# Optimization experiments

Hardware: AMD Instinct MI355X
Metric: run time of the kernel (lower is better)

## Reference

```python
import jax, jax.numpy as jnp
import numpy as np

N = 100000      # nodes
E = 1600000     # edges (before self-loops)
IN = 128        # in_channels
HID = 16        # hidden per head
HEADS = 8
OUT = 16        # out_channels (classes)
NEG_SLOPE = 0.2


def setup_inputs() -> dict:
    key = jax.random.key(0)
    ks = jax.random.split(key, 10)
    x = jax.random.normal(ks[0], (N, IN), jnp.float32)
    edge_index = jax.random.randint(ks[1], (2, E), 0, N, jnp.int32)
    g = lambda k, shape, fan: (jax.random.normal(k, shape, jnp.float32)
                               * (1.0 / np.sqrt(fan)).astype(np.float32))
    # layer 1: in -> heads*hid
    W1 = g(ks[2], (IN, HEADS * HID), IN)
    att_src1 = g(ks[3], (HEADS, HID), HID)
    att_dst1 = g(ks[4], (HEADS, HID), HID)
    b1 = jnp.zeros((HEADS * HID,), jnp.float32)
    # layer 2: heads*hid -> out, 1 head, concat=False
    W2 = g(ks[5], (HEADS * HID, OUT), HEADS * HID)
    att_src2 = g(ks[6], (1, OUT), OUT)
    att_dst2 = g(ks[7], (1, OUT), OUT)
    b2 = jnp.zeros((OUT,), jnp.float32)
    return dict(x=x, edge_index=edge_index, W1=W1, att_src1=att_src1,
                att_dst1=att_dst1, b1=b1, W2=W2, att_src2=att_src2,
                att_dst2=att_dst2, b2=b2)


def gat_conv(x, src, dst, W, a_src, a_dst, b, concat):
    """PyG-style GATConv (eval mode). src->dst message flow."""
    num_nodes = x.shape[0]
    H, C = a_src.shape
    h = (x @ W).reshape(num_nodes, H, C)                      # [N,H,C]
    # per-node attention halves, gathered to edges
    e = (h * a_src).sum(-1)[src] + (h * a_dst).sum(-1)[dst]   # [Etot,H]
    e = jax.nn.leaky_relu(e, NEG_SLOPE)
    # segment softmax over edges grouped by destination node
    emax = jax.ops.segment_max(e, dst, num_segments=num_nodes)    # [N,H]
    ee = jnp.exp(e - emax[dst])
    denom = jax.ops.segment_sum(ee, dst, num_segments=num_nodes)  # [N,H]
    alpha = ee / (denom[dst] + 1e-16)                              # [Etot,H]
    # weighted scatter-aggregate of source features
    msg = h[src] * alpha[:, :, None]                               # [Etot,H,C]
    out = jax.ops.segment_sum(msg, dst, num_segments=num_nodes)    # [N,H,C]
    out = out.reshape(num_nodes, H * C) if concat else out.mean(axis=1)
    return out + b


def reference(x, edge_index, W1, att_src1, att_dst1, b1,
              W2, att_src2, att_dst2, b2):
    # add self loops (PyG GATConv default)
    loop = jnp.arange(N, dtype=edge_index.dtype)
    src = jnp.concatenate([edge_index[0], loop])
    dst = jnp.concatenate([edge_index[1], loop])

    h = gat_conv(x, src, dst, W1, att_src1, att_dst1, b1, concat=True)
    embeddings = jax.nn.elu(h)
    logits = gat_conv(embeddings, src, dst, W2, att_src2, att_dst2, b2,
                      concat=False)
    return jax.nn.log_softmax(logits, axis=1), embeddings
```

## Files before the change

kernel.cpp:

```cpp
#include <hip/hip_runtime.h>
#include <hip/hip_bf16.h>
#include <math.h>

#define N_NODES 100000
#define E_EDGES 1600000
#define ETOT    (E_EDGES + N_NODES)
#define NEG     0.2f

#define SH        8
#define NBUCK     ((N_NODES + 255) >> 8)
#define BIN_TILE  4096
#define NBIN      ((E_EDGES + BIN_TILE - 1) / BIN_TILE)
#define CAP_B     5120

#define NMFMA     ((N_NODES + 63) / 64)
#define G_A       782
#define G_B       (NMFMA - G_A)

typedef __attribute__((ext_vector_type(8))) short bf16x8;
typedef __attribute__((ext_vector_type(4))) float f32x4;
typedef __attribute__((ext_vector_type(2))) short bf16p;

__device__ inline float lrelu(float x) { return x > 0.f ? x : NEG * x; }
__device__ inline float bflo(unsigned int b) { return __uint_as_float(b << 16); }
__device__ inline float bfhi(unsigned int b) { return __uint_as_float(b & 0xFFFF0000u); }
__device__ inline unsigned short f2bf(float f) {
    unsigned int u = __float_as_uint(f);
    return (unsigned short)((u + 0x7FFFu + ((u >> 16) & 1u)) >> 16);
}

__device__ inline float dot2bf(unsigned int wp, unsigned int hp, float c) {
#if __has_builtin(__builtin_amdgcn_fdot2_f32_bf16)
    return __builtin_amdgcn_fdot2_f32_bf16(__builtin_bit_cast(bf16p, wp),
                                           __builtin_bit_cast(bf16p, hp),
                                           c, false);
#else
    return fmaf(bflo(wp), bflo(hp), fmaf(bfhi(wp), bfhi(hp), c));
#endif
}

__global__ __launch_bounds__(256) void k_wt(const float* __restrict__ W,
                                            unsigned short* __restrict__ wtg) {
    int t = blockIdx.x * 256 + threadIdx.x;
    if (t >= 128 * 128) return;
    int n = t >> 7, k = t & 127;
    wtg[t] = f2bf(W[k * 128 + n]);
}

__global__ __launch_bounds__(256) void k_pack(const float* __restrict__ s1,
                                              unsigned short* __restrict__ s1b) {
    int n = blockIdx.x * 256 + threadIdx.x;
    if (n >= N_NODES) return;
    const float4* p = (const float4*)(s1 + (size_t)n * 8);
    float4 a = p[0], b = p[1];
    union { unsigned short u[8]; uint4 v; } o;
    o.u[0] = f2bf(a.x); o.u[1] = f2bf(a.y); o.u[2] = f2bf(a.z); o.u[3] = f2bf(a.w);
    o.u[4] = f2bf(b.x); o.u[5] = f2bf(b.y); o.u[6] = f2bf(b.z); o.u[7] = f2bf(b.w);
    *(uint4*)(s1b + (size_t)n * 8) = o.v;
}

__device__ __forceinline__ void gemm1_role(
    int n0, int t, unsigned short (*xb)[136],
    const float* __restrict__ x, const unsigned short* __restrict__ wtg,
    const float* __restrict__ asrc, const float* __restrict__ adst,
    __hip_bfloat16* __restrict__ h1b, float* __restrict__ s1,
    float* __restrict__ d1) {
#pragma unroll
    for (int i = 0; i < 8; ++i) {
        int i4 = t + i * 256;
        int r = i4 >> 5;
        int c = (i4 & 31) * 4;
        float4 v = make_float4(0.f, 0.f, 0.f, 0.f);
        if (n0 + r < N_NODES) v = *(const float4*)(x + (size_t)(n0 + r) * 128 + c);
        xb[r][c + 0] = f2bf(v.x);
        xb[r][c + 1] = f2bf(v.y);
        xb[r][c + 2] = f2bf(v.z);
        xb[r][c + 3] = f2bf(v.w);
    }
    __syncthreads();

    int l = t & 63, wv = t >> 6;
    int col = l & 15, q4 = l >> 4;
    int rbase = wv * 16;
    int koff = q4 * 8;

    bf16x8 a[4];
#pragma unroll
    for (int st = 0; st < 4; ++st)
        a[st] = *(const bf16x8*)&xb[rbase + col][st * 32 + koff];

    int nodeb = n0 + rbase + q4 * 4;
#pragma unroll
    for (int nt = 0; nt < 8; ++nt) {
        f32x4 acc = {0.f, 0.f, 0.f, 0.f};
        const unsigned short* wrow = wtg + (size_t)(nt * 16 + col) * 128 + koff;
#pragma unroll
        for (int st = 0; st < 4; ++st) {
            bf16x8 b = *(const bf16x8*)(wrow + st * 32);
            acc = __builtin_amdgcn_mfma_f32_16x16x32_bf16(a[st], b, acc, 0, 0, 0);
        }
        float as_v = asrc[nt * 16 + col];
        float ad_v = adst[nt * 16 + col];
#pragma unroll
        for (int r = 0; r < 4; ++r) {
            int node = nodeb + r;
            if (node < N_NODES)
                h1b[(size_t)node * 128 + nt * 16 + col] = __float2bfloat16(acc[r]);
            float ps = acc[r] * as_v, pd = acc[r] * ad_v;
#pragma unroll
            for (int ofs = 1; ofs < 16; ofs <<= 1) {
                ps += __shfl_xor(ps, ofs, 64);
                pd += __shfl_xor(pd, ofs, 64);
            }
            if (col == 0 && node < N_NODES) {
                s1[node * 8 + nt] = ps;
                d1[node * 8 + nt] = pd;
            }
        }
    }
}

union SmemBin {
    struct {
        int2 st[BIN_TILE];
        int  hist[NBUCK + 1];
        int  lstart[NBUCK];
        int  gbase[NBUCK];
        int  tsum[256];
    } b;
    unsigned short xb[64][136];
};

__global__ __launch_bounds__(256) void k_parBin(
    const int* __restrict__ src, const int* __restrict__ dst,
    int* __restrict__ gcur, int2* __restrict__ coo,
    const float* __restrict__ x, const unsigned short* __restrict__ wtg,
    const float* __restrict__ asrc, const float* __restrict__ adst,
    __hip_bfloat16* __restrict__ h1b, float* __restrict__ s1,
    float* __restrict__ d1) {
    __shared__ SmemBin sm;
    int bid = blockIdx.x, t = threadIdx.x;
    bool isBin = (bid % 3 == 0) && (bid / 3 < NBIN);
    if (!isBin) {
        int gid = bid - bid / 3 - 1;
        gemm1_role(gid * 64, t, sm.xb, x, wtg, asrc, adst, h1b, s1, d1);
        return;
    }
    int wb = bid / 3;
    int e0 = wb * BIN_TILE;
    int nE = min(BIN_TILE, E_EDGES - e0);
    for (int i = t; i <= NBUCK; i += 256) sm.b.hist[i] = 0;
    __syncthreads();
    for (int i = t; i < nE; i += 256)
        atomicAdd(&sm.b.hist[dst[e0 + i] >> SH], 1);
    __syncthreads();
    int i0 = 2 * t, i1 = 2 * t + 1;
    int h0 = (i0 < NBUCK) ? sm.b.hist[i0] : 0;
    int h1v = (i1 < NBUCK) ? sm.b.hist[i1] : 0;
    int s = h0 + h1v;
    sm.b.tsum[t] = s;
    __syncthreads();
    for (int ofs = 1; ofs < 256; ofs <<= 1) {
        int u = (t >= ofs) ? sm.b.tsum[t - ofs] : 0;
        __syncthreads();
        sm.b.tsum[t] += u;
        __syncthreads();
    }
    int pre = sm.b.tsum[t] - s;
    if (i0 < NBUCK) sm.b.hist[i0] = pre;
    if (i1 < NBUCK) sm.b.hist[i1] = pre + h0;
    if (t == 255) sm.b.hist[NBUCK] = sm.b.tsum[255];
    __syncthreads();
    for (int i = t; i < NBUCK; i += 256) {
        int st_ = sm.b.hist[i];
        int cnt = sm.b.hist[i + 1] - st_;
        sm.b.lstart[i] = st_;
        if (cnt > 0) sm.b.gbase[i] = i * CAP_B + atomicAdd(&gcur[i], cnt);
    }
    __syncthreads();
    for (int i = t; i < nE; i += 256) {
        int sv = src[e0 + i], dv = dst[e0 + i];
        int p = atomicAdd(&sm.b.hist[dv >> SH], 1);
        sm.b.st[p] = make_int2(sv, dv);
    }
    __syncthreads();
    for (int i = t; i < nE; i += 256) {
        int2 e = sm.b.st[i];
        int b2 = e.y >> SH;
        int slot = sm.b.gbase[b2] + (i - sm.b.lstart[b2]);
        slot = min(slot, (b2 + 1) * CAP_B - 1);
        coo[slot] = e;
    }
}

__global__ __launch_bounds__(256) void k_scanb(const int* __restrict__ gcur,
                                               int* __restrict__ bbase,
                                               int* __restrict__ off) {
    __shared__ int tsum[256];
    int t = threadIdx.x;
    int i0 = 2 * t, i1 = 2 * t + 1;
    int a = 0, b = 0;
    if (i0 < NBUCK) a = min(gcur[i0], CAP_B) + min(256, N_NODES - (i0 << SH));
    if (i1 < NBUCK) b = min(gcur[i1], CAP_B) + min(256, N_NODES - (i1 << SH));
    int s = a + b;
    tsum[t] = s;
    __syncthreads();
    for (int ofs = 1; ofs < 256; ofs <<= 1) {
        int u = (t >= ofs) ? tsum[t - ofs] : 0;
        __syncthreads();
        tsum[t] += u;
        __syncthreads();
    }
    int pre = tsum[t] - s;
    if (i0 < NBUCK) bbase[i0] = pre;
    if (i1 < NBUCK) bbase[i1] = pre + a;
    if (t == 0) off[N_NODES] = ETOT;
}

union SmemFine {
    struct {
        int ldeg[256];
        int lpre[256];
        int lsrc[CAP_B + 256];
    } f;
    unsigned short xb[64][136];
};

__global__ __launch_bounds__(256) void k_parFine(
    const int2* __restrict__ coo, const int* __restrict__ gcur,
    const int* __restrict__ bbase, int* __restrict__ off,
    int* __restrict__ csr,
    const float* __restrict__ x, const unsigned short* __restrict__ wtg,
    const float* __restrict__ asrc, const float* __restrict__ adst,
    __hip_bfloat16* __restrict__ h1b, float* __restrict__ s1,
    float* __restrict__ d1) {
    __shared__ SmemFine sm;
    int bid = blockIdx.x, t = threadIdx.x;
    bool isFine = (bid % 3 == 0) && (bid / 3 < NBUCK);
    if (!isFine) {
        int gid = bid - bid / 3 - 1;
        gemm1_role((G_A + gid) * 64, t, sm.xb, x, wtg, asrc, adst, h1b, s1, d1);
        return;
    }
    int b = bid / 3;
    int n0 = b << SH;
    int nn = min(256, N_NODES - n0);
    int ecnt = min(gcur[b], CAP_B);
    int base = bbase[b];
    const int2* seg = coo + (size_t)b * CAP_B;

    sm.f.ldeg[t] = 0;
    __syncthreads();
    for (int i = t; i < ecnt; i += 256)
        atomicAdd(&sm.f.ldeg[seg[i].y - n0], 1);
    __syncthreads();
    int d = (t < nn) ? sm.f.ldeg[t] + 1 : 0;
    sm.f.lpre[t] = d;
    __syncthreads();
    for (int ofs = 1; ofs < 256; ofs <<= 1) {
        int u = (t >= ofs) ? sm.f.lpre[t - ofs] : 0;
        __syncthreads();
        sm.f.lpre[t] += u;
        __syncthreads();
    }
    int myoff = sm.f.lpre[t] - d;
    __syncthreads();
    if (t < nn) {
        off[n0 + t] = base + myoff;
        sm.f.lsrc[myoff] = n0 + t;
        sm.f.ldeg[t] = myoff + 1;
    }
    __syncthreads();
    for (int i = t; i < ecnt; i += 256) {
        int2 e = seg[i];
        int p = atomicAdd(&sm.f.ldeg[e.y - n0], 1);
        sm.f.lsrc[p] = e.x;
    }
    __syncthreads();
    int tot = ecnt + nn;
    for (int i = t; i < tot; i += 256)
        csr[base + i] = sm.f.lsrc[i];
}

__global__ __launch_bounds__(256) void k_l1(
    const int* __restrict__ off, const int* __restrict__ csr,
    const unsigned short* __restrict__ s1b, const float* __restrict__ d1,
    const uint4* __restrict__ h1q, const float* __restrict__ b1,
    float* __restrict__ emb) {
    int t = threadIdx.x;
    int node = blockIdx.x * 4 + (t >> 6);
    int l = t & 63;
    int g = l >> 4, q = l & 15;
    int hb = q >> 1;
    int lo = off[node], hi = off[node + 1];
    float dvh = d1[node * 8 + hb];

    float acc[8];
#pragma unroll
    for (int c = 0; c < 8; ++c) acc[c] = 0.f;
    float den = 0.f;

    int idx = lo + g;
    bool have = (idx + 4 < hi);
    int sa = 0, sb = 0;
    uint4 ba = make_uint4(0, 0, 0, 0), bb = make_uint4(0, 0, 0, 0);
    float sva = 0.f, svb = 0.f;
    if (have) {
        sa = csr[idx]; sb = csr[idx + 4];
        ba = h1q[(size_t)sa * 16 + q];
        bb = h1q[(size_t)sb * 16 + q];
        sva = __uint_as_float((unsigned)s1b[(size_t)sa * 8 + hb] << 16);
        svb = __uint_as_float((unsigned)s1b[(size_t)sb * 8 + hb] << 16);
    }
    while (have) {
        int nidx = idx + 8;
        bool nhave = (nidx + 4 < hi);
        int na = 0, nb = 0;
        uint4 nba = make_uint4(0, 0, 0, 0), nbb = make_uint4(0, 0, 0, 0);
        float nsa = 0.f, nsb = 0.f;
        if (nhave) {
            na = csr[nidx]; nb = csr[nidx + 4];
            nba = h1q[(size_t)na * 16 + q];
            nbb = h1q[(size_t)nb * 16 + q];
            nsa = __uint_as_float((unsigned)s1b[(size_t)na * 8 + hb] << 16);
            nsb = __uint_as_float((unsigned)s1b[(size_t)nb * 8 + hb] << 16);
        }
        float w0 = __expf(lrelu(sva + dvh));
        float w1 = __expf(lrelu(svb + dvh));
        den += w0 + w1;
        unsigned int wp;
        asm("v_cvt_pk_bf16_f32 %0, %1, %2" : "=v"(wp) : "v"(w0), "v"(w1));
        unsigned int p0, p1;
        p0 = __builtin_amdgcn_perm(bb.x, ba.x, 0x05040100u);
        p1 = __builtin_amdgcn_perm(bb.x, ba.x, 0x07060302u);
        acc[0] = dot2bf(wp, p0, acc[0]);
        acc[1] = dot2bf(wp, p1, acc[1]);
        p0 = __builtin_amdgcn_perm(bb.y, ba.y, 0x05040100u);
        p1 = __builtin_amdgcn_perm(bb.y, ba.y, 0x07060302u);
        acc[2] = dot2bf(wp, p0, acc[2]);
        acc[3] = dot2bf(wp, p1, acc[3]);
        p0 = __builtin_amdgcn_perm(bb.z, ba.z, 0x05040100u);
        p1 = __builtin_amdgcn_perm(bb.z, ba.z, 0x07060302u);
        acc[4] = dot2bf(wp, p0, acc[4]);
        acc[5] = dot2bf(wp, p1, acc[5]);
        p0 = __builtin_amdgcn_perm(bb.w, ba.w, 0x05040100u);
        p1 = __builtin_amdgcn_perm(bb.w, ba.w, 0x07060302u);
        acc[6] = dot2bf(wp, p0, acc[6]);
        acc[7] = dot2bf(wp, p1, acc[7]);
        sa = na; sb = nb; ba = nba; bb = nbb; sva = nsa; svb = nsb;
        idx = nidx; have = nhave;
    }
    if (idx < hi) {
        int sc = csr[idx];
        uint4 bv = h1q[(size_t)sc * 16 + q];
        float sv = __uint_as_float((unsigned)s1b[(size_t)sc * 8 + hb] << 16);
        float w = __expf(lrelu(sv + dvh));
        den += w;
        acc[0] = fmaf(w, bflo(bv.x), acc[0]);
        acc[1] = fmaf(w, bfhi(bv.x), acc[1]);
        acc[2] = fmaf(w, bflo(bv.y), acc[2]);
        acc[3] = fmaf(w, bfhi(bv.y), acc[3]);
        acc[4] = fmaf(w, bflo(bv.z), acc[4]);
        acc[5] = fmaf(w, bfhi(bv.z), acc[5]);
        acc[6] = fmaf(w, bflo(bv.w), acc[6]);
        acc[7] = fmaf(w, bfhi(bv.w), acc[7]);
    }
#pragma unroll
    for (int c = 0; c < 8; ++c) {
        acc[c] += __shfl_xor(acc[c], 16, 64);
        acc[c] += __shfl_xor(acc[c], 32, 64);
    }
    den += __shfl_xor(den, 16, 64);
    den += __shfl_xor(den, 32, 64);

    if (l < 16) {
        float r = 1.f / den;
        float vv[8];
#pragma unroll
        for (int c = 0; c < 8; ++c) {
            float v = acc[c] * r + b1[8 * q + c];
            vv[c] = v > 0.f ? v : expm1f(v);
        }
        float4* ep = (float4*)(emb + (size_t)node * 128);
        ep[2 * q]     = make_float4(vv[0], vv[1], vv[2], vv[3]);
        ep[2 * q + 1] = make_float4(vv[4], vv[5], vv[6], vv[7]);
    }
}

__global__ __launch_bounds__(256) void k_gemm2(
    const float* __restrict__ emb, const float* __restrict__ W,
    const float* __restrict__ asrc, const float* __restrict__ adst,
    __hip_bfloat16* __restrict__ h2b, float* __restrict__ s2,
    float* __restrict__ d2) {
    __shared__ float xs[16][129];
    int n0 = blockIdx.x * 16;
    int t = threadIdx.x;
#pragma unroll
    for (int i = 0; i < 8; ++i) {
        int idx = t + i * 256;
        xs[idx >> 7][idx & 127] = emb[(long)n0 * 128 + idx];
    }
    __syncthreads();
    int j = t & 15, sub = t >> 4;
    float acc = 0.f;
    for (int k = 0; k < 128; ++k) acc = fmaf(xs[sub][k], W[k * 16 + j], acc);
    int n = n0 + sub;
    h2b[(long)n * 16 + j] = __float2bfloat16(acc);
    float ps = acc * asrc[j], pd = acc * adst[j];
#pragma unroll
    for (int off = 8; off; off >>= 1) {
        ps += __shfl_down(ps, off, 16);
        pd += __shfl_down(pd, off, 16);
    }
    if (j == 0) { s2[n] = ps; d2[n] = pd; }
}

__global__ __launch_bounds__(256) void k_l2(
    const int* __restrict__ off, const int* __restrict__ csr,
    const float* __restrict__ s2, const float* __restrict__ d2,
    const unsigned int* __restrict__ h2w, const float* __restrict__ b2,
    float* __restrict__ logits) {
    int t = threadIdx.x;
    int node = blockIdx.x * 4 + (t >> 6);
    int l = t & 63;
    int g = l >> 3, p = l & 7;
    int lo = off[node], hi = off[node + 1];
    float dv = d2[node];

    float ax = 0.f, ay = 0.f, den = 0.f;
    int idx = lo + g;
    int him = hi - 1;
    if (idx + 8 < hi) {
        int s0 = csr[idx], s1i = csr[idx + 8];
        unsigned int pa = h2w[(size_t)s0 * 8 + p];
        unsigned int pb = h2w[(size_t)s1i * 8 + p];
        float wa = s2[s0], wb = s2[s1i];
        int ia = csr[min(idx + 16, him)];
        int ib = csr[min(idx + 24, him)];
        while (true) {
            unsigned int npa = h2w[(size_t)ia * 8 + p];
            unsigned int npb = h2w[(size_t)ib * 8 + p];
            float nwa = s2[ia], nwb = s2[ib];
            int nia = csr[min(idx + 32, him)];
            int nib = csr[min(idx + 40, him)];
            float w0 = __expf(lrelu(wa + dv));
            float w1 = __expf(lrelu(wb + dv));
            den += w0 + w1;
            unsigned int wp;
            asm("v_cvt_pk_bf16_f32 %0, %1, %2" : "=v"(wp) : "v"(w0), "v"(w1));
            unsigned int p0 = __builtin_amdgcn_perm(pb, pa, 0x05040100u);
            unsigned int p1 = __builtin_amdgcn_perm(pb, pa, 0x07060302u);
            ax = dot2bf(wp, p0, ax);
            ay = dot2bf(wp, p1, ay);
            idx += 16;
            if (idx + 8 >= hi) break;
            pa = npa; pb = npb; wa = nwa; wb = nwb;
            ia = nia; ib = nib;
        }
    }
    if (idx < hi) {
        int s = csr[idx];
        float w = __expf(lrelu(s2[s] + dv));
        den += w;
        unsigned int bv = h2w[(size_t)s * 8 + p];
        ax = fmaf(w, bflo(bv), ax);
        ay = fmaf(w, bfhi(bv), ay);
    }
#pragma unroll
    for (int ofs = 8; ofs < 64; ofs <<= 1) {
        ax += __shfl_xor(ax, ofs, 64);
        ay += __shfl_xor(ay, ofs, 64);
        den += __shfl_xor(den, ofs, 64);
    }
    float r = 1.f / den;
    float v0 = ax * r + b2[2 * p], v1 = ay * r + b2[2 * p + 1];
    float mm = fmaxf(v0, v1);
#pragma unroll
    for (int ofs = 1; ofs < 8; ofs <<= 1) mm = fmaxf(mm, __shfl_xor(mm, ofs, 8));
    float sm = __expf(v0 - mm) + __expf(v1 - mm);
#pragma unroll
    for (int ofs = 1; ofs < 8; ofs <<= 1) sm += __shfl_xor(sm, ofs, 8);
    if (g == 0) {
        float ls = logf(sm);
        logits[node * 16 + 2 * p]     = v0 - mm - ls;
        logits[node * 16 + 2 * p + 1] = v1 - mm - ls;
    }
}

extern "C" void kernel_launch(void* const* d_in, const int* in_sizes, int n_in,
                              void* d_out, int out_size, void* d_ws, size_t ws_size,
                              hipStream_t stream) {
    const float* x   = (const float*)d_in[0];
    const int*   ei  = (const int*)d_in[1];
    const float* W1  = (const float*)d_in[2];
    const float* as1 = (const float*)d_in[3];
    const float* ad1 = (const float*)d_in[4];
    const float* b1  = (const float*)d_in[5];
    const float* W2  = (const float*)d_in[6];
    const float* as2 = (const float*)d_in[7];
    const float* ad2 = (const float*)d_in[8];
    const float* b2  = (const float*)d_in[9];

    float* out    = (float*)d_out;
    float* logits = out;
    float* emb    = out + (size_t)N_NODES * 16;

    float* ws    = (float*)d_ws;
    unsigned int* h1w = (unsigned int*)ws;
    int2*  coo   = (int2*)(h1w + (size_t)N_NODES * 64);
    float* s1    = (float*)(coo + (size_t)NBUCK * CAP_B);
    float* d1    = s1 + (size_t)N_NODES * 8;
    unsigned int* h2w = (unsigned int*)(d1 + (size_t)N_NODES * 8);
    float* s2    = (float*)(h2w + (size_t)N_NODES * 8);
    float* d2v   = s2 + (size_t)N_NODES;
    int*   offs  = (int*)(d2v + (size_t)N_NODES);
    int*   csr   = offs + N_NODES + 2;
    int*   gcur  = csr + ETOT;
    int*   bbase = gcur + NBUCK;
    unsigned short* wtg = (unsigned short*)(bbase + NBUCK);
    unsigned short* s1b = wtg + 128 * 128;

    const int* srcp = ei;
    const int* dstp = ei + E_EDGES;

    hipMemsetAsync(gcur, 0, (size_t)NBUCK * sizeof(int), stream);

    k_wt<<<64, 256, 0, stream>>>(W1, wtg);
    k_parBin<<<NBIN + G_A, 256, 0, stream>>>(srcp, dstp, gcur, coo,
                                             x, wtg, as1, ad1,
                                             (__hip_bfloat16*)h1w, s1, d1);
    k_scanb<<<1, 256, 0, stream>>>(gcur, bbase, offs);
    k_parFine<<<NBUCK + G_B, 256, 0, stream>>>(coo, gcur, bbase, offs, csr,
                                               x, wtg, as1, ad1,
                                               (__hip_bfloat16*)h1w, s1, d1);
    k_pack<<<(N_NODES + 255) / 256, 256, 0, stream>>>(s1, s1b);

    k_l1<<<N_NODES / 4, 256, 0, stream>>>(offs, csr, s1b, d1,
                                          (const uint4*)h1w, b1, emb);

    k_gemm2<<<N_NODES / 16, 256, 0, stream>>>(emb, W2, as2, ad2,
                                              (__hip_bfloat16*)h2w, s2, d2v);
    k_l2<<<N_NODES / 4, 256, 0, stream>>>(offs, csr, s2, d2v, h2w, b2, logits);
}
```

Baseline: 257.1 us.

## Fuse layer-2 GEMM into layer-1 aggregation, drop pack kernel, use wave scans

The layer-2 projection (emb @ W2 plus attention logits) is now computed inside the layer-1 aggregation kernel from a shared-memory copy of each node's embedding, so the separate GEMM2 kernel and its re-read of emb are gone. The GEMM1 role writes the source-attention scores directly as bf16, which removes the k_pack kernel and the fp32 s1 buffer. Block-wide prefix scans in the binning, bucket-scan and fine-sort kernels switch from shared-memory Hillis-Steele loops with many barriers to wave shuffle scans. The cost is extra shared memory and an extra barrier in k_l1, plus scalar FMA work there with W2 read from global memory.

```diff
diff --git a/kernel.cpp b/kernel.cpp
--- a/kernel.cpp
+++ b/kernel.cpp
@@ -39,6 +39,22 @@
 #endif
 }
 
+__device__ inline int exscan256(int v, int* wscr, int t) {
+    int lane = t & 63, wid = t >> 6;
+    int incl = v;
+#pragma unroll
+    for (int ofs = 1; ofs < 64; ofs <<= 1) {
+        int u = __shfl_up(incl, ofs, 64);
+        if (lane >= ofs) incl += u;
+    }
+    if (lane == 63) wscr[wid] = incl;
+    __syncthreads();
+    int wpre = 0;
+#pragma unroll
+    for (int w = 0; w < 4; ++w) wpre += (w < wid) ? wscr[w] : 0;
+    return wpre + incl - v;
+}
+
 __global__ __launch_bounds__(256) void k_wt(const float* __restrict__ W,
                                             unsigned short* __restrict__ wtg) {
     int t = blockIdx.x * 256 + threadIdx.x;
@@ -47,23 +63,11 @@
     wtg[t] = f2bf(W[k * 128 + n]);
 }
 
-__global__ __launch_bounds__(256) void k_pack(const float* __restrict__ s1,
-                                              unsigned short* __restrict__ s1b) {
-    int n = blockIdx.x * 256 + threadIdx.x;
-    if (n >= N_NODES) return;
-    const float4* p = (const float4*)(s1 + (size_t)n * 8);
-    float4 a = p[0], b = p[1];
-    union { unsigned short u[8]; uint4 v; } o;
-    o.u[0] = f2bf(a.x); o.u[1] = f2bf(a.y); o.u[2] = f2bf(a.z); o.u[3] = f2bf(a.w);
-    o.u[4] = f2bf(b.x); o.u[5] = f2bf(b.y); o.u[6] = f2bf(b.z); o.u[7] = f2bf(b.w);
-    *(uint4*)(s1b + (size_t)n * 8) = o.v;
-}
-
 __device__ __forceinline__ void gemm1_role(
     int n0, int t, unsigned short (*xb)[136],
     const float* __restrict__ x, const unsigned short* __restrict__ wtg,
     const float* __restrict__ asrc, const float* __restrict__ adst,
-    __hip_bfloat16* __restrict__ h1b, float* __restrict__ s1,
+    __hip_bfloat16* __restrict__ h1b, unsigned short* __restrict__ s1b,
     float* __restrict__ d1) {
 #pragma unroll
     for (int i = 0; i < 8; ++i) {
@@ -113,7 +117,7 @@
                 pd += __shfl_xor(pd, ofs, 64);
             }
             if (col == 0 && node < N_NODES) {
-                s1[node * 8 + nt] = ps;
+                s1b[node * 8 + nt] = f2bf(ps);
                 d1[node * 8 + nt] = pd;
             }
         }
@@ -126,7 +130,7 @@
         int  hist[NBUCK + 1];
         int  lstart[NBUCK];
         int  gbase[NBUCK];
-        int  tsum[256];
+        int  wscr[4];
     } b;
     unsigned short xb[64][136];
 };
@@ -136,14 +140,14 @@
     int* __restrict__ gcur, int2* __restrict__ coo,
     const float* __restrict__ x, const unsigned short* __restrict__ wtg,
     const float* __restrict__ asrc, const float* __restrict__ adst,
-    __hip_bfloat16* __restrict__ h1b, float* __restrict__ s1,
+    __hip_bfloat16* __restrict__ h1b, unsigned short* __restrict__ s1b,
     float* __restrict__ d1) {
     __shared__ SmemBin sm;
     int bid = blockIdx.x, t = threadIdx.x;
     bool isBin = (bid % 3 == 0) && (bid / 3 < NBIN);
     if (!isBin) {
         int gid = bid - bid / 3 - 1;
-        gemm1_role(gid * 64, t, sm.xb, x, wtg, asrc, adst, h1b, s1, d1);
+        gemm1_role(gid * 64, t, sm.xb, x, wtg, asrc, adst, h1b, s1b, d1);
         return;
     }
     int wb = bid / 3;
@@ -158,18 +162,11 @@
     int h0 = (i0 < NBUCK) ? sm.b.hist[i0] : 0;
     int h1v = (i1 < NBUCK) ? sm.b.hist[i1] : 0;
     int s = h0 + h1v;
-    sm.b.tsum[t] = s;
-    __syncthreads();
-    for (int ofs = 1; ofs < 256; ofs <<= 1) {
-        int u = (t >= ofs) ? sm.b.tsum[t - ofs] : 0;
-        __syncthreads();
-        sm.b.tsum[t] += u;
-        __syncthreads();
-    }
-    int pre = sm.b.tsum[t] - s;
+    int pre = exscan256(s, sm.b.wscr, t);
+    __syncthreads();
     if (i0 < NBUCK) sm.b.hist[i0] = pre;
     if (i1 < NBUCK) sm.b.hist[i1] = pre + h0;
-    if (t == 255) sm.b.hist[NBUCK] = sm.b.tsum[255];
+    if (t == 255) sm.b.hist[NBUCK] = pre + s;
     __syncthreads();
     for (int i = t; i < NBUCK; i += 256) {
         int st_ = sm.b.hist[i];
@@ -196,22 +193,14 @@
 __global__ __launch_bounds__(256) void k_scanb(const int* __restrict__ gcur,
                                                int* __restrict__ bbase,
                                                int* __restrict__ off) {
-    __shared__ int tsum[256];
+    __shared__ int wscr[4];
     int t = threadIdx.x;
     int i0 = 2 * t, i1 = 2 * t + 1;
     int a = 0, b = 0;
     if (i0 < NBUCK) a = min(gcur[i0], CAP_B) + min(256, N_NODES - (i0 << SH));
     if (i1 < NBUCK) b = min(gcur[i1], CAP_B) + min(256, N_NODES - (i1 << SH));
     int s = a + b;
-    tsum[t] = s;
-    __syncthreads();
-    for (int ofs = 1; ofs < 256; ofs <<= 1) {
-        int u = (t >= ofs) ? tsum[t - ofs] : 0;
-        __syncthreads();
-        tsum[t] += u;
-        __syncthreads();
-    }
-    int pre = tsum[t] - s;
+    int pre = exscan256(s, wscr, t);
     if (i0 < NBUCK) bbase[i0] = pre;
     if (i1 < NBUCK) bbase[i1] = pre + a;
     if (t == 0) off[N_NODES] = ETOT;
@@ -220,8 +209,8 @@
 union SmemFine {
     struct {
         int ldeg[256];
-        int lpre[256];
         int lsrc[CAP_B + 256];
+        int wscr[4];
     } f;
     unsigned short xb[64][136];
 };
@@ -232,14 +221,15 @@
     int* __restrict__ csr,
     const float* __restrict__ x, const unsigned short* __restrict__ wtg,
     const float* __restrict__ asrc, const float* __restrict__ adst,
-    __hip_bfloat16* __restrict__ h1b, float* __restrict__ s1,
+    __hip_bfloat16* __restrict__ h1b, unsigned short* __restrict__ s1b,
     float* __restrict__ d1) {
     __shared__ SmemFine sm;
     int bid = blockIdx.x, t = threadIdx.x;
     bool isFine = (bid % 3 == 0) && (bid / 3 < NBUCK);
     if (!isFine) {
         int gid = bid - bid / 3 - 1;
-        gemm1_role((G_A + gid) * 64, t, sm.xb, x, wtg, asrc, adst, h1b, s1, d1);
+        gemm1_role((G_A + gid) * 64, t, sm.xb, x, wtg, asrc, adst,
+                   h1b, s1b, d1);
         return;
     }
     int b = bid / 3;
@@ -255,15 +245,7 @@
         atomicAdd(&sm.f.ldeg[seg[i].y - n0], 1);
     __syncthreads();
     int d = (t < nn) ? sm.f.ldeg[t] + 1 : 0;
-    sm.f.lpre[t] = d;
-    __syncthreads();
-    for (int ofs = 1; ofs < 256; ofs <<= 1) {
-        int u = (t >= ofs) ? sm.f.lpre[t - ofs] : 0;
-        __syncthreads();
-        sm.f.lpre[t] += u;
-        __syncthreads();
-    }
-    int myoff = sm.f.lpre[t] - d;
+    int myoff = exscan256(d, sm.f.wscr, t);
     __syncthreads();
     if (t < nn) {
         off[n0 + t] = base + myoff;
@@ -286,9 +268,14 @@
     const int* __restrict__ off, const int* __restrict__ csr,
     const unsigned short* __restrict__ s1b, const float* __restrict__ d1,
     const uint4* __restrict__ h1q, const float* __restrict__ b1,
-    float* __restrict__ emb) {
+    float* __restrict__ emb,
+    const float* __restrict__ W2, const float* __restrict__ as2,
+    const float* __restrict__ ad2, unsigned short* __restrict__ h2s,
+    float* __restrict__ s2, float* __restrict__ d2v) {
+    __shared__ float esh[4][128];
     int t = threadIdx.x;
     int node = blockIdx.x * 4 + (t >> 6);
+    int wv = t >> 6;
     int l = t & 63;
     int g = l >> 4, q = l & 15;
     int hb = q >> 1;
@@ -380,39 +367,31 @@
         for (int c = 0; c < 8; ++c) {
             float v = acc[c] * r + b1[8 * q + c];
             vv[c] = v > 0.f ? v : expm1f(v);
+            esh[wv][8 * q + c] = vv[c];
         }
         float4* ep = (float4*)(emb + (size_t)node * 128);
         ep[2 * q]     = make_float4(vv[0], vv[1], vv[2], vv[3]);
         ep[2 * q + 1] = make_float4(vv[4], vv[5], vv[6], vv[7]);
     }
-}
-
-__global__ __launch_bounds__(256) void k_gemm2(
-    const float* __restrict__ emb, const float* __restrict__ W,
-    const float* __restrict__ asrc, const float* __restrict__ adst,
-    __hip_bfloat16* __restrict__ h2b, float* __restrict__ s2,
-    float* __restrict__ d2) {
-    __shared__ float xs[16][129];
-    int n0 = blockIdx.x * 16;
-    int t = threadIdx.x;
-#pragma unroll
-    for (int i = 0; i < 8; ++i) {
-        int idx = t + i * 256;
-        xs[idx >> 7][idx & 127] = emb[(long)n0 * 128 + idx];
-    }
-    __syncthreads();
-    int j = t & 15, sub = t >> 4;
-    float acc = 0.f;
-    for (int k = 0; k < 128; ++k) acc = fmaf(xs[sub][k], W[k * 16 + j], acc);
-    int n = n0 + sub;
-    h2b[(long)n * 16 + j] = __float2bfloat16(acc);
-    float ps = acc * asrc[j], pd = acc * adst[j];
-#pragma unroll
-    for (int off = 8; off; off >>= 1) {
-        ps += __shfl_down(ps, off, 16);
-        pd += __shfl_down(pd, off, 16);
-    }
-    if (j == 0) { s2[n] = ps; d2[n] = pd; }
+    __syncthreads();
+
+    int j = l & 15, part = l >> 4;
+    float o = 0.f;
+#pragma unroll
+    for (int cc = 0; cc < 32; ++cc) {
+        int c = part * 32 + cc;
+        o = fmaf(esh[wv][c], W2[c * 16 + j], o);
+    }
+    o += __shfl_xor(o, 16, 64);
+    o += __shfl_xor(o, 32, 64);
+    float ps = o * as2[j], pd = o * ad2[j];
+#pragma unroll
+    for (int ofs = 1; ofs < 16; ofs <<= 1) {
+        ps += __shfl_xor(ps, ofs, 16);
+        pd += __shfl_xor(pd, ofs, 16);
+    }
+    if (l < 16) h2s[(size_t)node * 16 + j] = f2bf(o);
+    if (l == 0) { s2[node] = ps; d2v[node] = pd; }
 }
 
 __global__ __launch_bounds__(256) void k_l2(
@@ -508,17 +487,16 @@
     float* ws    = (float*)d_ws;
     unsigned int* h1w = (unsigned int*)ws;
     int2*  coo   = (int2*)(h1w + (size_t)N_NODES * 64);
-    float* s1    = (float*)(coo + (size_t)NBUCK * CAP_B);
-    float* d1    = s1 + (size_t)N_NODES * 8;
-    unsigned int* h2w = (unsigned int*)(d1 + (size_t)N_NODES * 8);
-    float* s2    = (float*)(h2w + (size_t)N_NODES * 8);
+    unsigned short* s1b = (unsigned short*)(coo + (size_t)NBUCK * CAP_B);
+    float* d1    = (float*)(s1b + (size_t)N_NODES * 8);
+    unsigned short* h2s = (unsigned short*)(d1 + (size_t)N_NODES * 8);
+    float* s2    = (float*)(h2s + (size_t)N_NODES * 16);
     float* d2v   = s2 + (size_t)N_NODES;
     int*   offs  = (int*)(d2v + (size_t)N_NODES);
     int*   csr   = offs + N_NODES + 2;
     int*   gcur  = csr + ETOT;
     int*   bbase = gcur + NBUCK;
     unsigned short* wtg = (unsigned short*)(bbase + NBUCK);
-    unsigned short* s1b = wtg + 128 * 128;
 
     const int* srcp = ei;
     const int* dstp = ei + E_EDGES;
@@ -528,17 +506,16 @@
     k_wt<<<64, 256, 0, stream>>>(W1, wtg);
     k_parBin<<<NBIN + G_A, 256, 0, stream>>>(srcp, dstp, gcur, coo,
                                              x, wtg, as1, ad1,
-                                             (__hip_bfloat16*)h1w, s1, d1);
+                                             (__hip_bfloat16*)h1w, s1b, d1);
     k_scanb<<<1, 256, 0, stream>>>(gcur, bbase, offs);
     k_parFine<<<NBUCK + G_B, 256, 0, stream>>>(coo, gcur, bbase, offs, csr,
                                                x, wtg, as1, ad1,
-                                               (__hip_bfloat16*)h1w, s1, d1);
-    k_pack<<<(N_NODES + 255) / 256, 256, 0, stream>>>(s1, s1b);
+                                               (__hip_bfloat16*)h1w, s1b, d1);
 
     k_l1<<<N_NODES / 4, 256, 0, stream>>>(offs, csr, s1b, d1,
-                                          (const uint4*)h1w, b1, emb);
-
-    k_gemm2<<<N_NODES / 16, 256, 0, stream>>>(emb, W2, as2, ad2,
-                                              (__hip_bfloat16*)h2w, s2, d2v);
-    k_l2<<<N_NODES / 4, 256, 0, stream>>>(offs, csr, s2, d2v, h2w, b2, logits);
-}
+                                          (const uint4*)h1w, b1, emb,
+                                          W2, as2, ad2, h2s, s2, d2v);
+
+    k_l2<<<N_NODES / 4, 256, 0, stream>>>(offs, csr, s2, d2v,
+                                          (const unsigned int*)h2s, b2, logits);
+}
```

New measurement: 244.8 us. 4.8% less time.
